# Kernel tuning notes

Hardware: AMD Instinct MI355X
Metric: run time of the kernel (lower is better)

Reference implementation:

```python
import jax, jax.numpy as jnp
import numpy as np

V = 16000   # src/trg vocab
E = 512     # embedding dim (encoder_dim = decoder_dim)
H = 512     # hidden_size
L = 2       # n_layers
S = 128     # src len
T = 128     # trg len
B = 64      # batch


def _lstm_stack(x, Wih, Whh, bih, bhh, h0, c0):
    """Multi-layer LSTM, PyTorch gate order (i, f, g, o).
    x: [T, B, E]; Wih/Whh: [L, 4H, *]; bih/bhh: [L, 4H]; h0/c0: [L, B, H].
    Returns (outputs [T,B,H], hN [L,B,H], cN [L,B,H]). Dropout is eval-mode (identity)."""
    inp = x
    hs, cs = [], []
    for l in range(Wih.shape[0]):
        W1, W2 = Wih[l], Whh[l]
        b = bih[l] + bhh[l]
        def step(carry, xt, W1=W1, W2=W2, b=b):
            h, c = carry
            g = xt @ W1.T + h @ W2.T + b          # [B, 4H]
            i, f, gg, o = jnp.split(g, 4, axis=-1)
            c = jax.nn.sigmoid(f) * c + jax.nn.sigmoid(i) * jnp.tanh(gg)
            h = jax.nn.sigmoid(o) * jnp.tanh(c)
            return (h, c), h
        (h, c), ys = jax.lax.scan(step, (h0[l], c0[l]), inp)
        inp = ys
        hs.append(h)
        cs.append(c)
    return inp, jnp.stack(hs), jnp.stack(cs)


def setup_inputs() -> dict:
    key = jax.random.key(0)
    ks = jax.random.split(key, 16)
    u = lambda k, shape: jax.random.uniform(k, shape, jnp.float32, -0.08, 0.08)
    inp = {
        "src": jax.random.randint(ks[0], (S, B), 0, V),
        "trg": jax.random.randint(ks[1], (T, B), 0, V),
        "teacher_forcing_ratio": 1,
        "enc_emb": u(ks[2], (V, E)),
        "dec_emb": u(ks[3], (V, E)),
        "enc_Wih": jnp.stack([u(ks[4], (4 * H, E)), u(ks[5], (4 * H, H))]),
        "enc_Whh": u(ks[6], (L, 4 * H, H)),
        "enc_bih": u(ks[7], (L, 4 * H)),
        "enc_bhh": u(ks[8], (L, 4 * H)),
        "dec_Wih": jnp.stack([u(ks[9], (4 * H, E)), u(ks[10], (4 * H, H))]),
        "dec_Whh": u(ks[11], (L, 4 * H, H)),
        "dec_bih": u(ks[12], (L, 4 * H)),
        "dec_bhh": u(ks[13], (L, 4 * H)),
        "out_W": u(ks[14], (V, H)),
        "out_b": u(ks[15], (V,)),
    }
    return inp


def reference(src, trg, teacher_forcing_ratio, enc_emb, dec_emb,
              enc_Wih, enc_Whh, enc_bih, enc_bhh,
              dec_Wih, dec_Whh, dec_bih, dec_bhh, out_W, out_b):
    # Encoder: embed + 2-layer LSTM over src; keep final (h, c).
    zeros = jnp.zeros((L, B, H), enc_emb.dtype)
    _, h, c = _lstm_stack(enc_emb[src], enc_Wih, enc_Whh, enc_bih, enc_bhh, zeros, zeros)
    # Decoder: teacher_forcing_ratio=1 => input at step t is trg[t-1];
    # the per-step python loop collapses to one LSTM scan over trg[:-1].
    dec_in = dec_emb[trg[:-1]]                    # [T-1, B, E]
    ys, _, _ = _lstm_stack(dec_in, dec_Wih, dec_Whh, dec_bih, dec_bhh, h, c)
    logits = jnp.einsum('tbh,vh->tbv', ys, out_W) + out_b   # [T-1, B, V]
    # original: outputs[1:].view(-1, V)
    return logits.reshape(-1, V)
```

## Files before the change

### kernel.cpp

```cpp
#include <hip/hip_runtime.h>


typedef __attribute__((ext_vector_type(8))) short v8s;
typedef __attribute__((ext_vector_type(4))) short v4s;
typedef __attribute__((ext_vector_type(8))) _Float16 v8h;
typedef __attribute__((ext_vector_type(4))) float v4f;
typedef __attribute__((ext_vector_type(4))) unsigned int v4u;

#define AS1 __attribute__((address_space(1)))
#define AS3 __attribute__((address_space(3)))

__device__ __forceinline__ short f2h(float x) {
  _Float16 h = (_Float16)x;
  return __builtin_bit_cast(short, h);
}
__device__ __forceinline__ void gload16(const void* g, void* l) {
  __builtin_amdgcn_global_load_lds((const AS1 void*)g, (AS3 void*)l, 16, 0, 0);
}
__device__ __forceinline__ float sigf(float x) { return 1.f / (1.f + __expf(-x)); }
__device__ __forceinline__ float tanhfast(float x) { return 2.f / (1.f + __expf(-2.f * x)) - 1.f; }

__device__ __forceinline__ void ld16_sc1(v4u& d, const void* p) {
  asm volatile("global_load_dwordx4 %0, %1, off sc1" : "=v"(d) : "v"(p) : "memory");
}
__device__ __forceinline__ void ld16(v4u& d, const void* p) {
  asm volatile("global_load_dwordx4 %0, %1, off" : "=v"(d) : "v"(p));
}
__device__ __forceinline__ void spin_ge(unsigned* p, unsigned tgt) {
  while (__hip_atomic_load(p, __ATOMIC_RELAXED, __HIP_MEMORY_SCOPE_AGENT) < tgt)
    __builtin_amdgcn_s_sleep(1);
}

__global__ void conv_w(const float* __restrict__ in, short* __restrict__ out,
                       int rows, int ldo, int coloff, int reorder) {
  int i = blockIdx.x * 256 + threadIdx.x;
  if (i >= rows * 128) return;
  int r = i >> 7, k4 = (i & 127) * 4;
  int rr = reorder ? ((r & 511) * 4 + (r >> 9)) : r;
  float4 v = *(const float4*)(in + (size_t)r * 512 + k4);
  v4s s; s[0] = f2h(v.x); s[1] = f2h(v.y); s[2] = f2h(v.z); s[3] = f2h(v.w);
  *(v4s*)(out + (size_t)rr * ldo + coloff + k4) = s;
}

__global__ void conv_b(const float* __restrict__ a, const float* __restrict__ b,
                       float* __restrict__ o) {
  int r = blockIdx.x * 256 + threadIdx.x;
  if (r < 2048) o[(r & 511) * 4 + (r >> 9)] = a[r] + b[r];
}

__global__ void embed_k(const int* __restrict__ ids, const float* __restrict__ emb,
                        short* __restrict__ out, int nvalid) {
  int row = blockIdx.x;
  int e = threadIdx.x * 2;
  float2 v = make_float2(0.f, 0.f);
  if (row < nvalid) {
    int id = ids[row];
    v = *(const float2*)(emb + (size_t)id * 512 + e);
  }
  unsigned pack = ((unsigned)(unsigned short)f2h(v.y) << 16) | (unsigned short)f2h(v.x);
  *(unsigned*)(out + (size_t)row * 512 + e) = pack;
}

__global__ void zero_k(short* p, int n) {
  int i = blockIdx.x * 256 + threadIdx.x;
  if (i < n) p[i] = 0;
}

#define GF_BIAS 2
#define GF_GUARDM 4

__global__ __launch_bounds__(256, 2) void gemm_bt(
    const short* __restrict__ Am, const short* __restrict__ Bm,
    const float* __restrict__ bias, float* __restrict__ Cm,
    int M, int N, int K, int ldc, int flags) {
  __shared__ short lA[128 * 64];
  __shared__ short lB[128 * 64];
  const int tid = threadIdx.x, lane = tid & 63, wave = tid >> 6;
  const int wm = wave >> 1, wn = wave & 1;
  const int tm = blockIdx.y, tn = blockIdx.x;
  v4f acc[4][4] = {};
  const short* Abase = Am + (size_t)tm * 128 * K;
  const short* Bbase = Bm + (size_t)tn * 128 * K;

  for (int kt = 0; kt < K; kt += 64) {
    __syncthreads();
#pragma unroll
    for (int i2 = 0; i2 < 4; ++i2) {
      int c = (wave * 4 + i2) * 64 + lane;
      int row = c >> 3, ch = c & 7;
      int sch = ch ^ (row & 7);
      gload16(Abase + (size_t)row * K + kt + sch * 8, (char*)lA + (wave * 4 + i2) * 1024);
      gload16(Bbase + (size_t)row * K + kt + sch * 8, (char*)lB + (wave * 4 + i2) * 1024);
    }
    asm volatile("s_waitcnt vmcnt(0)" ::: "memory");
    __syncthreads();
#pragma unroll
    for (int kc = 0; kc < 2; ++kc) {
      v8h af[4], bh[4];
#pragma unroll
      for (int mt = 0; mt < 4; ++mt) {
        int row = wm * 64 + mt * 16 + (lane & 15);
        af[mt] = *(const v8h*)((const char*)lA + row * 128 +
                               ((kc * 64 + (lane >> 4) * 16) ^ ((row & 7) << 4)));
      }
#pragma unroll
      for (int nt = 0; nt < 4; ++nt) {
        int row = wn * 64 + nt * 16 + (lane & 15);
        bh[nt] = *(const v8h*)((const char*)lB + row * 128 +
                               ((kc * 64 + (lane >> 4) * 16) ^ ((row & 7) << 4)));
      }
#pragma unroll
      for (int mt = 0; mt < 4; ++mt)
#pragma unroll
        for (int nt = 0; nt < 4; ++nt)
          acc[mt][nt] = __builtin_amdgcn_mfma_f32_16x16x32_f16(af[mt], bh[nt], acc[mt][nt], 0, 0, 0);
    }
  }

  const int rbase = tm * 128 + wm * 64 + (lane >> 4) * 4;
  const int cbase = tn * 128 + wn * 64 + (lane & 15);
#pragma unroll
  for (int mt = 0; mt < 4; ++mt) {
#pragma unroll
    for (int nt = 0; nt < 4; ++nt) {
      int gc = cbase + nt * 16;
      float bv = (flags & GF_BIAS) ? bias[gc] : 0.f;
#pragma unroll
      for (int rg = 0; rg < 4; ++rg) {
        int gr = rbase + mt * 16 + rg;
        if ((flags & GF_GUARDM) && gr >= M) continue;
        Cm[(size_t)gr * ldc + gc] = acc[mt][nt][rg] + bv;
      }
    }
  }
}

struct PipeArgs {
  const short* W0e;
  const short* W0d;
  const short* W1e;
  const short* W1d;
  const short* X;
  const float* b0e;
  const float* b0d;
  const float* b1e;
  const float* b1d;
  short* h0;
  short* h1;
  unsigned* done0;
  unsigned* done1;
  int Tenc, Ttot;
};

#define PRE_LD 68
#define SLOT 32768

__global__ __launch_bounds__(256, 1) void lstm_pipe(PipeArgs A) {
  __shared__ __align__(16) short Wlds[64 * 1024];
  __shared__ __align__(16) float pre[64 * PRE_LD];
  __shared__ __align__(16) short hsm[64 * 16];
  const int tid = threadIdx.x, lane = tid & 63, wave = tid >> 6;
  const int w = blockIdx.x, layer = w >> 5, wl = w & 31;

  auto stage = [&](const short* Wsrc) {
    for (int i = tid * 8; i < 64 * 1024; i += 256 * 8) {
      int row = i >> 10, k = i & 1023;
      v8s v = *(const v8s*)(Wsrc + (size_t)row * 1024 + k);
      *(v8s*)((char*)Wlds + row * 2048 + ((k * 2) ^ ((row & 7) << 4))) = v;
    }
  };
  stage(((layer ? A.W1e : A.W0e)) + (size_t)(wl * 64) * 1024);

  const int uu = tid & 15, bq0 = tid >> 4;
  const float* bpe = (layer ? A.b1e : A.b0e) + wl * 64 + uu * 4;
  const float* bpd = (layer ? A.b1d : A.b0d) + wl * 64 + uu * 4;
  const float be0 = bpe[0], be1 = bpe[1], be2 = bpe[2], be3 = bpe[3];
  const float bd0 = bpd[0], bd1 = bpd[1], bd2 = bpd[2], bd3 = bpd[3];
  float creg[4] = {0.f, 0.f, 0.f, 0.f};
  unsigned* own = layer ? A.done1 : A.done0;

  const int arow = wave * 16 + (lane & 15);
  const int koff = (lane >> 4) * 8;
  __syncthreads();

  for (int t = 0; t < A.Ttot; ++t) {
    if (t == A.Tenc) {
      stage((layer ? A.W1d : A.W0d) + (size_t)(wl * 64) * 1024);
      __syncthreads();
    }

    if (layer) {
      if (tid == 0) spin_ge(A.done0 + (size_t)(t + 1) * 32, 32u);
      __syncthreads();
    }
    const short* s1 = layer ? (A.h0 + (size_t)(t + 1) * SLOT)
                            : (A.X + (size_t)t * SLOT);
    const short* p1 = s1 + (size_t)arow * 512 + koff;
    v4u fa[16];
    if (layer) {
#pragma unroll
      for (int kc = 0; kc < 16; ++kc) ld16_sc1(fa[kc], p1 + kc * 32);
    } else {
#pragma unroll
      for (int kc = 0; kc < 16; ++kc) ld16(fa[kc], p1 + kc * 32);
    }
    asm volatile("s_waitcnt vmcnt(0)" ::: "memory");
    __builtin_amdgcn_sched_barrier(0);
    v4f acc[4] = {};
#pragma unroll
    for (int kc = 0; kc < 16; ++kc) {
      v8h af = __builtin_bit_cast(v8h, fa[kc]);
      int kg = kc * 32 + koff;
#pragma unroll
      for (int nt = 0; nt < 4; ++nt) {
        int wrow = nt * 16 + (lane & 15);
        v8h bh = *(const v8h*)((const char*)Wlds + wrow * 2048 +
                               ((kg * 2) ^ ((wrow & 7) << 4)));
        acc[nt] = __builtin_amdgcn_mfma_f32_16x16x32_f16(af, bh, acc[nt], 0, 0, 0);
      }
    }

    if (tid == 0 && t > 0) spin_ge(own + (size_t)t * 32, 32u);
    __syncthreads();
    const short* s2 = (layer ? A.h1 : A.h0) + (size_t)t * SLOT;
    const short* p2 = s2 + (size_t)arow * 512 + koff;
    v4u fb[16];
#pragma unroll
    for (int kc = 0; kc < 16; ++kc) ld16_sc1(fb[kc], p2 + kc * 32);
    asm volatile("s_waitcnt vmcnt(0)" ::: "memory");
    __builtin_amdgcn_sched_barrier(0);
#pragma unroll
    for (int kc = 0; kc < 16; ++kc) {
      v8h af = __builtin_bit_cast(v8h, fb[kc]);
      int kg = (kc + 16) * 32 + koff;
#pragma unroll
      for (int nt = 0; nt < 4; ++nt) {
        int wrow = nt * 16 + (lane & 15);
        v8h bh = *(const v8h*)((const char*)Wlds + wrow * 2048 +
                               ((kg * 2) ^ ((wrow & 7) << 4)));
        acc[nt] = __builtin_amdgcn_mfma_f32_16x16x32_f16(af, bh, acc[nt], 0, 0, 0);
      }
    }
#pragma unroll
    for (int nt = 0; nt < 4; ++nt)
#pragma unroll
      for (int rg = 0; rg < 4; ++rg)
        pre[(wave * 16 + (lane >> 4) * 4 + rg) * PRE_LD + nt * 16 + (lane & 15)] = acc[nt][rg];
    __syncthreads();

    {
      const bool enc = t < A.Tenc;
#pragma unroll
      for (int q = 0; q < 4; ++q) {
        int b = q * 16 + bq0;
        v4f gv = *(const v4f*)(&pre[b * PRE_LD + uu * 4]);
        float g0 = gv[0] + (enc ? be0 : bd0);
        float g1 = gv[1] + (enc ? be1 : bd1);
        float g2 = gv[2] + (enc ? be2 : bd2);
        float g3 = gv[3] + (enc ? be3 : bd3);
        float c = sigf(g1) * creg[q] + sigf(g0) * tanhfast(g2);
        creg[q] = c;
        float h = sigf(g3) * tanhfast(c);
        hsm[b * 16 + uu] = f2h(h);
      }
    }
    __syncthreads();

    if (tid < 128) {
      int b = tid >> 1, half = tid & 1;
      v4u d = *(const v4u*)(&hsm[b * 16 + half * 8]);
      short* dst = (layer ? A.h1 : A.h0) + (size_t)(t + 1) * SLOT
                   + b * 512 + wl * 16 + half * 8;
      asm volatile("global_store_dwordx4 %0, %1, off sc1" :: "v"(dst), "v"(d) : "memory");
    }
    asm volatile("s_waitcnt vmcnt(0)" ::: "memory");
    __syncthreads();
    if (tid == 0)
      __hip_atomic_fetch_add(own + (size_t)(t + 1) * 32, 1u,
                             __ATOMIC_RELAXED, __HIP_MEMORY_SCOPE_AGENT);
  }
}

extern "C" void kernel_launch(void* const* d_in, const int* in_sizes, int n_in,
                              void* d_out, int out_size, void* d_ws, size_t ws_size,
                              hipStream_t stream) {
  (void)in_sizes; (void)n_in; (void)out_size; (void)ws_size;
  const int* src = (const int*)d_in[0];
  const int* trg = (const int*)d_in[1];
  const float* enc_emb = (const float*)d_in[3];
  const float* dec_emb = (const float*)d_in[4];
  const float* enc_Wih = (const float*)d_in[5];
  const float* enc_Whh = (const float*)d_in[6];
  const float* enc_bih = (const float*)d_in[7];
  const float* enc_bhh = (const float*)d_in[8];
  const float* dec_Wih = (const float*)d_in[9];
  const float* dec_Whh = (const float*)d_in[10];
  const float* dec_bih = (const float*)d_in[11];
  const float* dec_bhh = (const float*)d_in[12];
  const float* out_W = (const float*)d_in[13];
  const float* out_b = (const float*)d_in[14];

  char* p = (char*)d_ws;
  auto alloc = [&](size_t sz) { char* r = p; p += (sz + 255) & ~(size_t)255; return r; };
  short* H0 = (short*)alloc((size_t)256 * SLOT * 2);
  short* H1 = (short*)alloc((size_t)257 * SLOT * 2);
  short* W0e = (short*)alloc((size_t)2048 * 1024 * 2);
  short* W0d = (short*)alloc((size_t)2048 * 1024 * 2);
  short* W1e = (short*)alloc((size_t)2048 * 1024 * 2);
  short* W1d = (short*)alloc((size_t)2048 * 1024 * 2);
  short* XO = (short*)alloc((size_t)255 * SLOT * 2);
  float* bE0 = (float*)alloc(2048 * 4);
  float* bE1 = (float*)alloc(2048 * 4);
  float* bD0 = (float*)alloc(2048 * 4);
  float* bD1 = (float*)alloc(2048 * 4);
  unsigned* done0 = (unsigned*)alloc(256 * 32 * 4);
  unsigned* done1 = (unsigned*)alloc(256 * 32 * 4);

  zero_k<<<128, 256, 0, stream>>>(H0, 32768);
  zero_k<<<128, 256, 0, stream>>>(H1, 32768);
  zero_k<<<128, 256, 0, stream>>>(H1 + (size_t)256 * SLOT, 32768);
  zero_k<<<128, 256, 0, stream>>>((short*)done0, 32768);

  conv_w<<<1024, 256, 0, stream>>>(enc_Wih, W0e, 2048, 1024, 0, 1);
  conv_w<<<1024, 256, 0, stream>>>(enc_Whh, W0e, 2048, 1024, 512, 1);
  conv_w<<<1024, 256, 0, stream>>>(dec_Wih, W0d, 2048, 1024, 0, 1);
  conv_w<<<1024, 256, 0, stream>>>(dec_Whh, W0d, 2048, 1024, 512, 1);
  conv_w<<<1024, 256, 0, stream>>>(enc_Wih + (size_t)2048 * 512, W1e, 2048, 1024, 0, 1);
  conv_w<<<1024, 256, 0, stream>>>(enc_Whh + (size_t)2048 * 512, W1e, 2048, 1024, 512, 1);
  conv_w<<<1024, 256, 0, stream>>>(dec_Wih + (size_t)2048 * 512, W1d, 2048, 1024, 0, 1);
  conv_w<<<1024, 256, 0, stream>>>(dec_Whh + (size_t)2048 * 512, W1d, 2048, 1024, 512, 1);
  conv_b<<<8, 256, 0, stream>>>(enc_bih, enc_bhh, bE0);
  conv_b<<<8, 256, 0, stream>>>(enc_bih + 2048, enc_bhh + 2048, bE1);
  conv_b<<<8, 256, 0, stream>>>(dec_bih, dec_bhh, bD0);
  conv_b<<<8, 256, 0, stream>>>(dec_bih + 2048, dec_bhh + 2048, bD1);

  embed_k<<<8192, 256, 0, stream>>>(src, enc_emb, XO, 8192);
  embed_k<<<8128, 256, 0, stream>>>(trg, dec_emb, XO + (size_t)8192 * 512, 8128);

  PipeArgs pa = {W0e, W0d, W1e, W1d, XO, bE0, bD0, bE1, bD1,
                 H0, H1, done0, done1, 128, 255};
  lstm_pipe<<<64, 256, 0, stream>>>(pa);

  short* outWb = XO;
  conv_w<<<8000, 256, 0, stream>>>(out_W, outWb, 16000, 512, 0, 0);

  gemm_bt<<<dim3(125, 64), 256, 0, stream>>>(H1 + (size_t)129 * SLOT, outWb, out_b,
                                             (float*)d_out, 8128, 16000, 512, 16000,
                                             GF_BIAS | GF_GUARDM);
}
```

Measured before the change: 2.373 ms.

## Reorder gate rows so LSTM cell update runs from MFMA registers

Weight and bias rows are permuted so each 16-column MFMA tile holds one gate (i, f, g, o) for the same 16 hidden units. The cell update can then read the accumulators directly, which removes the shared-memory staging buffer and one block barrier per step. Both wait conditions are now checked up front, and the input and recurrent loads are issued together as one batch of 32 loads. The cost is that the input projection no longer overlaps the wait on the own layer's previous step, and register pressure rises from the 32 outstanding loads.

```diff
diff --git a/kernel.cpp b/kernel.cpp
--- a/kernel.cpp
+++ b/kernel.cpp
@@ -36,7 +36,7 @@
   int i = blockIdx.x * 256 + threadIdx.x;
   if (i >= rows * 128) return;
   int r = i >> 7, k4 = (i & 127) * 4;
-  int rr = reorder ? ((r & 511) * 4 + (r >> 9)) : r;
+  int rr = reorder ? (((r >> 4) & 31) * 64 + (r >> 9) * 16 + (r & 15)) : r;
   float4 v = *(const float4*)(in + (size_t)r * 512 + k4);
   v4s s; s[0] = f2h(v.x); s[1] = f2h(v.y); s[2] = f2h(v.z); s[3] = f2h(v.w);
   *(v4s*)(out + (size_t)rr * ldo + coloff + k4) = s;
@@ -45,7 +45,7 @@
 __global__ void conv_b(const float* __restrict__ a, const float* __restrict__ b,
                        float* __restrict__ o) {
   int r = blockIdx.x * 256 + threadIdx.x;
-  if (r < 2048) o[(r & 511) * 4 + (r >> 9)] = a[r] + b[r];
+  if (r < 2048) o[((r >> 4) & 31) * 64 + (r >> 9) * 16 + (r & 15)] = a[r] + b[r];
 }
 
 __global__ void embed_k(const int* __restrict__ ids, const float* __restrict__ emb,
@@ -152,12 +152,10 @@
   int Tenc, Ttot;
 };
 
-#define PRE_LD 68
 #define SLOT 32768
 
 __global__ __launch_bounds__(256, 1) void lstm_pipe(PipeArgs A) {
   __shared__ __align__(16) short Wlds[64 * 1024];
-  __shared__ __align__(16) float pre[64 * PRE_LD];
   __shared__ __align__(16) short hsm[64 * 16];
   const int tid = threadIdx.x, lane = tid & 63, wave = tid >> 6;
   const int w = blockIdx.x, layer = w >> 5, wl = w & 31;
@@ -169,18 +167,21 @@
       *(v8s*)((char*)Wlds + row * 2048 + ((k * 2) ^ ((row & 7) << 4))) = v;
     }
   };
-  stage(((layer ? A.W1e : A.W0e)) + (size_t)(wl * 64) * 1024);
-
-  const int uu = tid & 15, bq0 = tid >> 4;
-  const float* bpe = (layer ? A.b1e : A.b0e) + wl * 64 + uu * 4;
-  const float* bpd = (layer ? A.b1d : A.b0d) + wl * 64 + uu * 4;
-  const float be0 = bpe[0], be1 = bpe[1], be2 = bpe[2], be3 = bpe[3];
-  const float bd0 = bpd[0], bd1 = bpd[1], bd2 = bpd[2], bd3 = bpd[3];
+  stage((layer ? A.W1e : A.W0e) + (size_t)(wl * 64) * 1024);
+
+  const int uu = lane & 15;
+  float beV[4], bdV[4];
+#pragma unroll
+  for (int g = 0; g < 4; ++g) {
+    beV[g] = (layer ? A.b1e : A.b0e)[wl * 64 + g * 16 + uu];
+    bdV[g] = (layer ? A.b1d : A.b0d)[wl * 64 + g * 16 + uu];
+  }
   float creg[4] = {0.f, 0.f, 0.f, 0.f};
   unsigned* own = layer ? A.done1 : A.done0;
 
-  const int arow = wave * 16 + (lane & 15);
+  const int arow = wave * 16 + uu;
   const int koff = (lane >> 4) * 8;
+  const size_t aoff = (size_t)arow * 512 + koff;
   __syncthreads();
 
   for (int t = 0; t < A.Ttot; ++t) {
@@ -189,79 +190,63 @@
       __syncthreads();
     }
 
+    if (tid == 0) {
+      if (layer) {
+        spin_ge(A.done0 + (size_t)(t + 1) * 32, 32u);
+        if (t > 0) spin_ge(A.done1 + (size_t)t * 32, 32u);
+      } else if (t > 0) {
+        spin_ge(A.done0 + (size_t)t * 32, 32u);
+      }
+    }
+    __syncthreads();
+
+    const short* p1 = (layer ? (A.h0 + (size_t)(t + 1) * SLOT)
+                             : (A.X + (size_t)t * SLOT)) + aoff;
+    const short* p2 = ((layer ? A.h1 : A.h0) + (size_t)t * SLOT) + aoff;
+    v4u fl[32];
     if (layer) {
-      if (tid == 0) spin_ge(A.done0 + (size_t)(t + 1) * 32, 32u);
-      __syncthreads();
-    }
-    const short* s1 = layer ? (A.h0 + (size_t)(t + 1) * SLOT)
-                            : (A.X + (size_t)t * SLOT);
-    const short* p1 = s1 + (size_t)arow * 512 + koff;
-    v4u fa[16];
-    if (layer) {
-#pragma unroll
-      for (int kc = 0; kc < 16; ++kc) ld16_sc1(fa[kc], p1 + kc * 32);
+#pragma unroll
+      for (int kc = 0; kc < 16; ++kc) ld16_sc1(fl[kc], p1 + kc * 32);
     } else {
 #pragma unroll
-      for (int kc = 0; kc < 16; ++kc) ld16(fa[kc], p1 + kc * 32);
-    }
+      for (int kc = 0; kc < 16; ++kc) ld16(fl[kc], p1 + kc * 32);
+    }
+#pragma unroll
+    for (int kc = 0; kc < 16; ++kc) ld16_sc1(fl[16 + kc], p2 + kc * 32);
     asm volatile("s_waitcnt vmcnt(0)" ::: "memory");
     __builtin_amdgcn_sched_barrier(0);
+
     v4f acc[4] = {};
 #pragma unroll
-    for (int kc = 0; kc < 16; ++kc) {
-      v8h af = __builtin_bit_cast(v8h, fa[kc]);
+    for (int kc = 0; kc < 32; ++kc) {
+      v8h af = __builtin_bit_cast(v8h, fl[kc]);
       int kg = kc * 32 + koff;
 #pragma unroll
       for (int nt = 0; nt < 4; ++nt) {
-        int wrow = nt * 16 + (lane & 15);
+        int wrow = nt * 16 + uu;
         v8h bh = *(const v8h*)((const char*)Wlds + wrow * 2048 +
                                ((kg * 2) ^ ((wrow & 7) << 4)));
         acc[nt] = __builtin_amdgcn_mfma_f32_16x16x32_f16(af, bh, acc[nt], 0, 0, 0);
       }
     }
 
-    if (tid == 0 && t > 0) spin_ge(own + (size_t)t * 32, 32u);
-    __syncthreads();
-    const short* s2 = (layer ? A.h1 : A.h0) + (size_t)t * SLOT;
-    const short* p2 = s2 + (size_t)arow * 512 + koff;
-    v4u fb[16];
-#pragma unroll
-    for (int kc = 0; kc < 16; ++kc) ld16_sc1(fb[kc], p2 + kc * 32);
-    asm volatile("s_waitcnt vmcnt(0)" ::: "memory");
-    __builtin_amdgcn_sched_barrier(0);
-#pragma unroll
-    for (int kc = 0; kc < 16; ++kc) {
-      v8h af = __builtin_bit_cast(v8h, fb[kc]);
-      int kg = (kc + 16) * 32 + koff;
-#pragma unroll
-      for (int nt = 0; nt < 4; ++nt) {
-        int wrow = nt * 16 + (lane & 15);
-        v8h bh = *(const v8h*)((const char*)Wlds + wrow * 2048 +
-                               ((kg * 2) ^ ((wrow & 7) << 4)));
-        acc[nt] = __builtin_amdgcn_mfma_f32_16x16x32_f16(af, bh, acc[nt], 0, 0, 0);
-      }
-    }
-#pragma unroll
-    for (int nt = 0; nt < 4; ++nt)
-#pragma unroll
-      for (int rg = 0; rg < 4; ++rg)
-        pre[(wave * 16 + (lane >> 4) * 4 + rg) * PRE_LD + nt * 16 + (lane & 15)] = acc[nt][rg];
-    __syncthreads();
-
     {
       const bool enc = t < A.Tenc;
-#pragma unroll
-      for (int q = 0; q < 4; ++q) {
-        int b = q * 16 + bq0;
-        v4f gv = *(const v4f*)(&pre[b * PRE_LD + uu * 4]);
-        float g0 = gv[0] + (enc ? be0 : bd0);
-        float g1 = gv[1] + (enc ? be1 : bd1);
-        float g2 = gv[2] + (enc ? be2 : bd2);
-        float g3 = gv[3] + (enc ? be3 : bd3);
-        float c = sigf(g1) * creg[q] + sigf(g0) * tanhfast(g2);
-        creg[q] = c;
+      const float b0v = enc ? beV[0] : bdV[0];
+      const float b1v = enc ? beV[1] : bdV[1];
+      const float b2v = enc ? beV[2] : bdV[2];
+      const float b3v = enc ? beV[3] : bdV[3];
+#pragma unroll
+      for (int rg = 0; rg < 4; ++rg) {
+        float g0 = acc[0][rg] + b0v;
+        float g1 = acc[1][rg] + b1v;
+        float g2 = acc[2][rg] + b2v;
+        float g3 = acc[3][rg] + b3v;
+        float c = sigf(g1) * creg[rg] + sigf(g0) * tanhfast(g2);
+        creg[rg] = c;
         float h = sigf(g3) * tanhfast(c);
-        hsm[b * 16 + uu] = f2h(h);
+        int bb = wave * 16 + ((lane >> 4) << 2) + rg;
+        hsm[bb * 16 + uu] = f2h(h);
       }
     }
     __syncthreads();
```

Measured after the change: 2.900 ms. 1.22x slower.
